# Optimization experiments

Measured on AMD Instinct MI355X. Metric: run time of the kernel, lower is better.

## Reference

```python
import jax, jax.numpy as jnp
import numpy as np

NUM_HEADS = 12
EPSILON = 1e-6
SCORE_SCALE = 1.0


def setup_inputs() -> dict:
    key = jax.random.key(0)
    ks = jax.random.split(key, 5)
    B, L, E = 2, 2048, 768
    x = jax.random.normal(ks[0], (B, L, E), dtype=jnp.float32)
    attention_mask = jnp.ones((B, L), dtype=jnp.int32)
    # linear params (lecun-ish scale)
    Wqkv = jax.random.normal(ks[1], (E, 3 * E), dtype=jnp.float32) / np.sqrt(E)
    bqkv = jnp.zeros((3 * E,), dtype=jnp.float32)
    Wout = jax.random.normal(ks[2], (E, E), dtype=jnp.float32) / np.sqrt(E)
    bout = jnp.zeros((E,), dtype=jnp.float32)
    return {"x": x, "attention_mask": attention_mask, "Wqkv": Wqkv,
            "bqkv": bqkv, "Wout": Wout, "bout": bout}


def reference(x, attention_mask, Wqkv, bqkv, Wout, bout):
    B, L, E = x.shape
    H = NUM_HEADS
    D = E // H
    qkv = x @ Wqkv + bqkv                      # [B,L,3E]
    q, k, v = jnp.split(qkv, 3, axis=-1)
    q = q.reshape(B, L, H, D).transpose(0, 2, 1, 3)  # [B,H,L,D]
    k = k.reshape(B, L, H, D).transpose(0, 2, 1, 3)
    v = v.reshape(B, L, H, D).transpose(0, 2, 1, 3)

    dot = jnp.einsum('bhid,bhjd->bhij', q, k)        # [B,H,L,L]
    q_sq = jnp.sum(q * q, axis=-1)[..., :, None]     # [B,H,L,1]
    k_sq = jnp.sum(k * k, axis=-1)[..., None, :]     # [B,H,1,L]
    scores = (dot * dot) / (q_sq + k_sq - 2.0 * dot + EPSILON)
    scores = scores * SCORE_SCALE

    pad = attention_mask[:, None, None, :]           # [B,1,1,L]
    scores = jnp.where(pad == 1, scores, jnp.finfo(scores.dtype).min)

    attn = jax.nn.softmax(scores, axis=-1)
    out = jnp.einsum('bhij,bhjd->bhid', attn, v)     # [B,H,L,D]
    out = out.transpose(0, 2, 1, 3).reshape(B, L, E)
    return out @ Wout + bout
```

## Files before the change

kernel.cpp:

```cpp
#include <hip/hip_runtime.h>
#include <hip/hip_bf16.h>
#include <cstdint>
#include <cstddef>


typedef __bf16 bf16_t;
typedef __bf16 bf16x8 __attribute__((ext_vector_type(8)));
typedef __bf16 bf16x4 __attribute__((ext_vector_type(4)));
typedef float floatx4 __attribute__((ext_vector_type(4)));

#define DEVI static __device__ __forceinline__

#define Bc 2
#define Lc 2048
#define Ec 768
#define Hc 12
#define Dc 64
#define N3c 2304
#define Mc 4096
#define ROWSc (Bc * Hc * Lc)

DEVI void glds16(const bf16_t* g, bf16_t* l) {
  __builtin_amdgcn_global_load_lds(
      (const __attribute__((address_space(1))) void*)g,
      (__attribute__((address_space(3))) void*)l, 16, 0, 0);
}


__global__ __launch_bounds__(256) void k_cvt(const float* __restrict__ in,
                                             bf16_t* __restrict__ out, int n) {
  int i = (blockIdx.x * 256 + threadIdx.x) * 4;
  if (i >= n) return;
  float4 v = *(const float4*)(in + i);
  bf16x4 o;
  o[0] = (bf16_t)v.x; o[1] = (bf16_t)v.y; o[2] = (bf16_t)v.z; o[3] = (bf16_t)v.w;
  *(bf16x4*)(out + i) = o;
}

__global__ __launch_bounds__(256) void k_tc(const float* __restrict__ in,
                                            bf16_t* __restrict__ out, int R, int C) {
  __shared__ float tile[32][33];
  int c0 = blockIdx.x * 32, r0 = blockIdx.y * 32;
  int tx = threadIdx.x, ty = threadIdx.y;
  #pragma unroll
  for (int i = 0; i < 32; i += 8)
    tile[ty + i][tx] = in[(size_t)(r0 + ty + i) * C + c0 + tx];
  __syncthreads();
  #pragma unroll
  for (int i = 0; i < 32; i += 8)
    out[(size_t)(c0 + ty + i) * R + r0 + tx] = (bf16_t)tile[tx][ty + i];
}


DEVI void gemm_core(const bf16_t* __restrict__ A, const bf16_t* __restrict__ Bt,
                    bf16_t* lA, bf16_t* lB, int m0, int n0, floatx4 (&acc)[4][4]) {
  const int tid = threadIdx.x, wave = tid >> 6, lane = tid & 63;
  const int wm = (wave >> 1) * 64, wn = (wave & 1) * 64;
  const int lrow = lane >> 2, lseg = lane & 3;
  const int quad = lane >> 4, r16 = lane & 15;
  for (int kk = 0; kk < 768; kk += 32) {
    glds16(A  + (size_t)(m0 + wave * 32      + lrow) * 768 + kk + lseg * 8, lA + (wave * 32) * 32);
    glds16(A  + (size_t)(m0 + wave * 32 + 16 + lrow) * 768 + kk + lseg * 8, lA + (wave * 32 + 16) * 32);
    glds16(Bt + (size_t)(n0 + wave * 32      + lrow) * 768 + kk + lseg * 8, lB + (wave * 32) * 32);
    glds16(Bt + (size_t)(n0 + wave * 32 + 16 + lrow) * 768 + kk + lseg * 8, lB + (wave * 32 + 16) * 32);
    __syncthreads();
    bf16x8 af[4], bv[4];
    #pragma unroll
    for (int mi = 0; mi < 4; mi++)
      af[mi] = *(const bf16x8*)(lA + (wm + mi * 16 + r16) * 32 + quad * 8);
    #pragma unroll
    for (int ni = 0; ni < 4; ni++)
      bv[ni] = *(const bf16x8*)(lB + (wn + ni * 16 + r16) * 32 + quad * 8);
    #pragma unroll
    for (int mi = 0; mi < 4; mi++)
      #pragma unroll
      for (int ni = 0; ni < 4; ni++)
        acc[mi][ni] = __builtin_amdgcn_mfma_f32_16x16x32_bf16(af[mi], bv[ni], acc[mi][ni], 0, 0, 0);
    __syncthreads();
  }
}

__global__ __launch_bounds__(256) void k_gemm_qkv(
    const bf16_t* __restrict__ A, const bf16_t* __restrict__ Bt,
    const float* __restrict__ bias,
    bf16_t* __restrict__ Qo, bf16_t* __restrict__ Ko, bf16_t* __restrict__ Vo) {
  __shared__ bf16_t lA[128 * 32];
  __shared__ bf16_t lB[128 * 32];
  const int m0 = blockIdx.y * 128, n0 = blockIdx.x * 128;
  const int tid = threadIdx.x, wave = tid >> 6, lane = tid & 63;
  const int wm = (wave >> 1) * 64, wn = (wave & 1) * 64;
  const int quad = lane >> 4, r16 = lane & 15;
  floatx4 acc[4][4] = {};
  gemm_core(A, Bt, lA, lB, m0, n0, acc);

  const int sec = n0 / 768;
  bf16_t* dst = (sec == 0) ? Qo : ((sec == 1) ? Ko : Vo);
  #pragma unroll
  for (int ni = 0; ni < 4; ni++) {
    const int n = n0 + wn + ni * 16 + r16;
    const int nn = n - sec * 768;
    const int h = nn >> 6, d = nn & 63;
    const float bvs = bias[n];
    #pragma unroll
    for (int mi = 0; mi < 4; mi++) {
      #pragma unroll
      for (int reg = 0; reg < 4; reg++) {
        const int m = m0 + wm + mi * 16 + quad * 4 + reg;
        const int b = m >> 11, l = m & 2047;
        const float v = acc[mi][ni][reg] + bvs;
        dst[(((size_t)(b * Hc + h)) * Lc + l) * Dc + d] = (bf16_t)v;
      }
    }
  }
}

__global__ __launch_bounds__(256) void k_gemm_out(
    const bf16_t* __restrict__ A, const bf16_t* __restrict__ Bt,
    const float* __restrict__ bias, float* __restrict__ out) {
  __shared__ bf16_t lA[128 * 32];
  __shared__ bf16_t lB[128 * 32];
  const int m0 = blockIdx.y * 128, n0 = blockIdx.x * 128;
  const int tid = threadIdx.x, wave = tid >> 6, lane = tid & 63;
  const int wm = (wave >> 1) * 64, wn = (wave & 1) * 64;
  const int quad = lane >> 4, r16 = lane & 15;
  floatx4 acc[4][4] = {};
  gemm_core(A, Bt, lA, lB, m0, n0, acc);
  #pragma unroll
  for (int ni = 0; ni < 4; ni++) {
    const int n = n0 + wn + ni * 16 + r16;
    const float bvs = bias[n];
    #pragma unroll
    for (int mi = 0; mi < 4; mi++) {
      #pragma unroll
      for (int reg = 0; reg < 4; reg++) {
        const int m = m0 + wm + mi * 16 + quad * 4 + reg;
        out[(size_t)m * Ec + n] = acc[mi][ni][reg] + bvs;
      }
    }
  }
}

__global__ __launch_bounds__(256) void k_sq(const bf16_t* __restrict__ Q,
                                            const bf16_t* __restrict__ K,
                                            const int* __restrict__ mask,
                                            float* __restrict__ qsq, float* __restrict__ ksq,
                                            float* __restrict__ mbias) {
  const int row = blockIdx.x * 256 + threadIdx.x;
  const bf16x8* q = (const bf16x8*)(Q + (size_t)row * 64);
  const bf16x8* k = (const bf16x8*)(K + (size_t)row * 64);
  float sq = 0.f, sk = 0.f;
  #pragma unroll
  for (int c = 0; c < 8; c++) {
    bf16x8 vq = q[c], vk = k[c];
    #pragma unroll
    for (int j = 0; j < 8; j++) {
      float a = (float)vq[j]; sq += a * a;
      float b = (float)vk[j]; sk += b * b;
    }
  }
  qsq[row] = sq;
  ksq[row] = sk + 1e-6f;
  const int bh = row >> 11, l = row & 2047;
  if (bh == 0 || bh == Hc) {
    const int b = bh / Hc;
    mbias[b * Lc + l] = (mask[b * Lc + l] == 1) ? 0.f : -1e30f;
  }
}

__global__ __launch_bounds__(256) void k_vt(const bf16_t* __restrict__ V,
                                            bf16_t* __restrict__ VT) {
  __shared__ bf16_t t[64][72];
  const int gid = blockIdx.x;
  const int bh = gid >> 5, j0 = (gid & 31) * 64;
  const int tid = threadIdx.x;
  const bf16_t* Vh = V + ((size_t)bh * Lc) * Dc;
  bf16_t* VTh = VT + ((size_t)bh * Dc) * Lc;
  #pragma unroll
  for (int it = 0; it < 2; ++it) {
    int c = tid + it * 256;
    int j = c >> 3, seg = c & 7;
    *(bf16x8*)&t[j][seg * 8] = *(const bf16x8*)(Vh + (size_t)(j0 + j) * 64 + seg * 8);
  }
  __syncthreads();
  #pragma unroll
  for (int it = 0; it < 2; ++it) {
    int c = tid + it * 256;
    int d = c >> 3, jseg = c & 7;
    bf16x8 o;
    #pragma unroll
    for (int u = 0; u < 8; u++) o[u] = t[jseg * 8 + u][d];
    *(bf16x8*)(VTh + (size_t)d * Lc + j0 + jseg * 8) = o;
  }
}

__global__ __launch_bounds__(256) void k_attn(
    const bf16_t* __restrict__ Q, const bf16_t* __restrict__ K,
    const bf16_t* __restrict__ VT, const float* __restrict__ qsq,
    const float* __restrict__ ksq, const float* __restrict__ mbias,
    bf16_t* __restrict__ AO) {
  __shared__ bf16_t lK[2][4096];
  __shared__ bf16_t lV[2][4096];
  __shared__ bf16_t lP[4][16 * 72];
  const int gid0 = blockIdx.x;
  const int gid = (gid0 & 7) * 96 + (gid0 >> 3);
  const int bh = gid >> 5, qt = gid & 31;
  const int b = bh / Hc;
  const int h = bh - b * Hc;
  const int tid = threadIdx.x, wave = tid >> 6, lane = tid & 63;
  const int quad = lane >> 4, r16 = lane & 15;
  const int q0 = qt * 64 + wave * 16;
  const bf16_t* Qh = Q + ((size_t)bh * Lc) * Dc;
  const bf16_t* Kh = K + ((size_t)bh * Lc) * Dc;
  const bf16_t* VTh = VT + ((size_t)bh * Dc) * Lc;
  const float* qsqh = qsq + bh * Lc;
  const float* ksqh = ksq + bh * Lc;
  const float* mbb = mbias + b * Lc;
  bf16_t* myP = &lP[wave][0];

  const int p0 = wave * 64 + lane;
  const int srow = p0 >> 3;
  const int sj = (p0 & 7) ^ (srow & 7);
  const bf16_t* kg0 = Kh + (size_t)srow * 64 + sj * 8;
  const bf16_t* kg1 = kg0 + 32 * 64;
  const bf16_t* vg0 = VTh + (size_t)srow * Lc + sj * 8;
  const bf16_t* vg1 = vg0 + 32 * Lc;
  const int ld0 = wave * 64 * 8, ld1 = (256 + wave * 64) * 8;

  const int sl0 = ((quad ^ (r16 & 7)) * 8);
  const int sl1 = sl0 ^ 32;

  bf16x8 qf0 = *(const bf16x8*)(Qh + (size_t)(q0 + r16) * 64 + quad * 8);
  bf16x8 qf1 = *(const bf16x8*)(Qh + (size_t)(q0 + r16) * 64 + 32 + quad * 8);
  const float qs = qsqh[q0 + r16];
  float mi = -1e30f, li = 0.f;
  floatx4 of[4] = {};

  glds16(kg0, &lK[0][ld0]);
  glds16(kg1, &lK[0][ld1]);
  glds16(vg0, &lV[0][ld0]);
  glds16(vg1, &lV[0][ld1]);
  kg0 += 4096; kg1 += 4096; vg0 += 64; vg1 += 64;
  __syncthreads();

  const int nt = Lc / 64;
  for (int t = 0; t < nt; t++) {
    const int cur = t & 1;
    if (t + 1 < nt) {
      const int nxt = cur ^ 1;
      glds16(kg0, &lK[nxt][ld0]);
      glds16(kg1, &lK[nxt][ld1]);
      glds16(vg0, &lV[nxt][ld0]);
      glds16(vg1, &lV[nxt][ld1]);
      kg0 += 4096; kg1 += 4096; vg0 += 64; vg1 += 64;
    }
    const int kt = t * 64;
    float4 ks4[4], mb4[4];
    #pragma unroll
    for (int c = 0; c < 4; c++) {
      ks4[c] = *(const float4*)(ksqh + kt + c * 16 + quad * 4);
      mb4[c] = *(const float4*)(mbb + kt + c * 16 + quad * 4);
    }
    floatx4 dot[4];
    #pragma unroll
    for (int c = 0; c < 4; c++) {
      const int rbase = (c * 16 + r16) * 64;
      bf16x8 kf0 = *(const bf16x8*)(&lK[cur][rbase + sl0]);
      bf16x8 kf1 = *(const bf16x8*)(&lK[cur][rbase + sl1]);
      floatx4 a = {};
      a = __builtin_amdgcn_mfma_f32_16x16x32_bf16(kf0, qf0, a, 0, 0, 0);
      a = __builtin_amdgcn_mfma_f32_16x16x32_bf16(kf1, qf1, a, 0, 0, 0);
      dot[c] = a;
    }
    float rmax = -1e30f;
    #pragma unroll
    for (int c = 0; c < 4; c++) {
      #pragma unroll
      for (int reg = 0; reg < 4; reg++) {
        const float dd = dot[c][reg];
        const float kss = ((const float*)&ks4[c])[reg];
        const float mbv = ((const float*)&mb4[c])[reg];
        const float den = __builtin_fmaf(dd, -2.f, qs + kss);
        const float sc = __builtin_fmaf((dd * 1.44269504f) * dd,
                                        __builtin_amdgcn_rcpf(den), mbv);
        dot[c][reg] = sc;
        rmax = fmaxf(rmax, sc);
      }
    }
    rmax = fmaxf(rmax, __shfl_xor(rmax, 16));
    rmax = fmaxf(rmax, __shfl_xor(rmax, 32));
    if (!__all(rmax <= mi + 11.5416f)) {
      const float mnew = fmaxf(mi, rmax);
      const float alpha = exp2f(mi - mnew);
      li *= alpha;
      #pragma unroll
      for (int t4 = 0; t4 < 4; t4++) {
        #pragma unroll
        for (int reg = 0; reg < 4; reg++) of[t4][reg] *= alpha;
      }
      mi = mnew;
    }
    float psum = 0.f;
    #pragma unroll
    for (int c = 0; c < 4; c++) {
      bf16x4 pk;
      #pragma unroll
      for (int reg = 0; reg < 4; reg++) {
        const float p = exp2f(dot[c][reg] - mi);
        psum += p;
        pk[reg] = (bf16_t)p;
      }
      *(bf16x4*)(myP + r16 * 72 + c * 16 + quad * 4) = pk;
    }
    psum += __shfl_xor(psum, 16);
    psum += __shfl_xor(psum, 32);
    li += psum;
    bf16x8 pf0 = *(const bf16x8*)(myP + r16 * 72 + quad * 8);
    bf16x8 pf1 = *(const bf16x8*)(myP + r16 * 72 + 32 + quad * 8);
    #pragma unroll
    for (int t4 = 0; t4 < 4; t4++) {
      const int rbase = (t4 * 16 + r16) * 64;
      bf16x8 vf0 = *(const bf16x8*)(&lV[cur][rbase + sl0]);
      bf16x8 vf1 = *(const bf16x8*)(&lV[cur][rbase + sl1]);
      of[t4] = __builtin_amdgcn_mfma_f32_16x16x32_bf16(vf0, pf0, of[t4], 0, 0, 0);
      of[t4] = __builtin_amdgcn_mfma_f32_16x16x32_bf16(vf1, pf1, of[t4], 0, 0, 0);
    }
    __syncthreads();
  }
  const float inv = (li > 0.f) ? __builtin_amdgcn_rcpf(li) : 0.f;
  bf16_t* aor = AO + ((size_t)(b * Lc + q0 + r16)) * Ec + h * 64;
  #pragma unroll
  for (int t4 = 0; t4 < 4; t4++) {
    bf16x4 o;
    #pragma unroll
    for (int reg = 0; reg < 4; reg++) o[reg] = (bf16_t)(of[t4][reg] * inv);
    *(bf16x4*)(aor + t4 * 16 + quad * 4) = o;
  }
}


extern "C" void kernel_launch(void* const* d_in, const int* in_sizes, int n_in,
                              void* d_out, int out_size, void* d_ws, size_t ws_size,
                              hipStream_t stream) {
  const float* x    = (const float*)d_in[0];
  const int*   mask = (const int*)d_in[1];
  const float* Wqkv = (const float*)d_in[2];
  const float* bqkv = (const float*)d_in[3];
  const float* Wout = (const float*)d_in[4];
  const float* bout = (const float*)d_in[5];
  float* out = (float*)d_out;

  auto al = [](size_t x) { return (x + 255) & ~(size_t)255; };
  char* ws = (char*)d_ws;
  size_t off = 0;
  auto carve = [&](size_t bytes) -> char* {
    char* p = ws + off;
    off += al(bytes);
    return p;
  };
  bf16_t* WoT = (bf16_t*)carve((size_t)Ec * Ec * 2);
  bf16_t* Qb  = (bf16_t*)carve((size_t)ROWSc * Dc * 2);
  bf16_t* Kb  = (bf16_t*)carve((size_t)ROWSc * Dc * 2);
  bf16_t* VTb = (bf16_t*)carve((size_t)ROWSc * Dc * 2);
  bf16_t* AOb = (bf16_t*)carve((size_t)Mc * Ec * 2);
  float*  qsq = (float*)carve((size_t)ROWSc * 4);
  float*  ksq = (float*)carve((size_t)ROWSc * 4);
  float*  mbias = (float*)carve((size_t)Bc * Lc * 4);
  const size_t uni = off;
  bf16_t* xb  = (bf16_t*)(ws + uni);
  bf16_t* WqT = (bf16_t*)(ws + uni + al((size_t)Mc * Ec * 2));
  bf16_t* Vb  = (bf16_t*)(ws + uni + al((size_t)Mc * Ec * 2) + al((size_t)N3c * Ec * 2));
  (void)in_sizes; (void)n_in; (void)out_size; (void)ws_size;

  k_cvt<<<(Mc * Ec / 4 + 255) / 256, 256, 0, stream>>>(x, xb, Mc * Ec);
  k_tc<<<dim3(N3c / 32, Ec / 32), dim3(32, 8), 0, stream>>>(Wqkv, WqT, Ec, N3c);
  k_tc<<<dim3(Ec / 32, Ec / 32), dim3(32, 8), 0, stream>>>(Wout, WoT, Ec, Ec);
  k_gemm_qkv<<<dim3(N3c / 128, Mc / 128), 256, 0, stream>>>(xb, WqT, bqkv, Qb, Kb, Vb);
  k_sq<<<ROWSc / 256, 256, 0, stream>>>(Qb, Kb, mask, qsq, ksq, mbias);
  k_vt<<<ROWSc / 64, 256, 0, stream>>>(Vb, VTb);
  k_attn<<<dim3(ROWSc / 64), 256, 0, stream>>>(Qb, Kb, VTb, qsq, ksq, mbias, AOb);
  k_gemm_out<<<dim3(Ec / 128, Mc / 128), 256, 0, stream>>>(AOb, WoT, bout, out);
}
```

Baseline: 219.4 us.

## Merge prep kernels, prefetch ksq/mask per tile, defer softmax reductions

Merges the x conversion and both weight transposes into one launch, and merges the squared-norm/mask kernel with the V transpose into another, cutting five launches to two. In the attention loop, the ksq and mask-bias loads for the next key tile are issued one iteration early. The row-max cross-lane shuffle now runs only inside the rescale branch, and the row-sum shuffle moves to after the loop. This trims per-iteration shuffles and load latency at the cost of extra registers, and the merged kernels use branching block roles.

Result: faster. 210.4 us (-4.1%).

```diff
diff --git a/kernel.cpp b/kernel.cpp
--- a/kernel.cpp
+++ b/kernel.cpp
@@ -26,22 +26,27 @@
       (__attribute__((address_space(3))) void*)l, 16, 0, 0);
 }
 
-
-__global__ __launch_bounds__(256) void k_cvt(const float* __restrict__ in,
-                                             bf16_t* __restrict__ out, int n) {
-  int i = (blockIdx.x * 256 + threadIdx.x) * 4;
-  if (i >= n) return;
-  float4 v = *(const float4*)(in + i);
-  bf16x4 o;
-  o[0] = (bf16_t)v.x; o[1] = (bf16_t)v.y; o[2] = (bf16_t)v.z; o[3] = (bf16_t)v.w;
-  *(bf16x4*)(out + i) = o;
-}
-
-__global__ __launch_bounds__(256) void k_tc(const float* __restrict__ in,
-                                            bf16_t* __restrict__ out, int R, int C) {
+__global__ __launch_bounds__(256) void k_prep(
+    const float* __restrict__ x, bf16_t* __restrict__ xb,
+    const float* __restrict__ Wqkv, bf16_t* __restrict__ WqT,
+    const float* __restrict__ Wout, bf16_t* __restrict__ WoT) {
   __shared__ float tile[32][33];
-  int c0 = blockIdx.x * 32, r0 = blockIdx.y * 32;
-  int tx = threadIdx.x, ty = threadIdx.y;
+  const int bid = blockIdx.x, tid = threadIdx.x;
+  if (bid < 3072) {
+    const int i = (bid * 256 + tid) * 4;
+    float4 v = *(const float4*)(x + i);
+    bf16x4 o;
+    o[0] = (bf16_t)v.x; o[1] = (bf16_t)v.y; o[2] = (bf16_t)v.z; o[3] = (bf16_t)v.w;
+    *(bf16x4*)(xb + i) = o;
+    return;
+  }
+  const float* in; bf16_t* out; int C, local;
+  if (bid < 4800) { local = bid - 3072; in = Wqkv; out = WqT; C = N3c; }
+  else            { local = bid - 4800; in = Wout; out = WoT; C = Ec;  }
+  const int R = Ec;
+  const int nbx = C / 32;
+  const int c0 = (local % nbx) * 32, r0 = (local / nbx) * 32;
+  const int tx = tid & 31, ty = tid >> 5;
   #pragma unroll
   for (int i = 0; i < 32; i += 8)
     tile[ty + i][tx] = in[(size_t)(r0 + ty + i) * C + c0 + tx];
@@ -140,46 +145,46 @@
   }
 }
 
-__global__ __launch_bounds__(256) void k_sq(const bf16_t* __restrict__ Q,
-                                            const bf16_t* __restrict__ K,
-                                            const int* __restrict__ mask,
-                                            float* __restrict__ qsq, float* __restrict__ ksq,
-                                            float* __restrict__ mbias) {
-  const int row = blockIdx.x * 256 + threadIdx.x;
-  const bf16x8* q = (const bf16x8*)(Q + (size_t)row * 64);
-  const bf16x8* k = (const bf16x8*)(K + (size_t)row * 64);
-  float sq = 0.f, sk = 0.f;
-  #pragma unroll
-  for (int c = 0; c < 8; c++) {
-    bf16x8 vq = q[c], vk = k[c];
-    #pragma unroll
-    for (int j = 0; j < 8; j++) {
-      float a = (float)vq[j]; sq += a * a;
-      float b = (float)vk[j]; sk += b * b;
-    }
-  }
-  qsq[row] = sq;
-  ksq[row] = sk + 1e-6f;
-  const int bh = row >> 11, l = row & 2047;
-  if (bh == 0 || bh == Hc) {
-    const int b = bh / Hc;
-    mbias[b * Lc + l] = (mask[b * Lc + l] == 1) ? 0.f : -1e30f;
-  }
-}
-
-__global__ __launch_bounds__(256) void k_vt(const bf16_t* __restrict__ V,
-                                            bf16_t* __restrict__ VT) {
-  __shared__ bf16_t t[64][72];
-  const int gid = blockIdx.x;
+__global__ __launch_bounds__(256) void k_prep2(
+    const bf16_t* __restrict__ Q, const bf16_t* __restrict__ K,
+    const int* __restrict__ mask,
+    float* __restrict__ qsq, float* __restrict__ ksq,
+    float* __restrict__ mbias,
+    const bf16_t* __restrict__ V, bf16_t* __restrict__ VT) {
+  __shared__ bf16_t tb[64][72];
+  const int bid = blockIdx.x, tid = threadIdx.x;
+  if (bid < 192) {
+    const int row = bid * 256 + tid;
+    const bf16x8* q = (const bf16x8*)(Q + (size_t)row * 64);
+    const bf16x8* k = (const bf16x8*)(K + (size_t)row * 64);
+    float sq = 0.f, sk = 0.f;
+    #pragma unroll
+    for (int c = 0; c < 8; c++) {
+      bf16x8 vq = q[c], vk = k[c];
+      #pragma unroll
+      for (int j = 0; j < 8; j++) {
+        float a = (float)vq[j]; sq += a * a;
+        float b = (float)vk[j]; sk += b * b;
+      }
+    }
+    qsq[row] = sq;
+    ksq[row] = sk + 1e-6f;
+    const int bh = row >> 11, l = row & 2047;
+    if (bh == 0 || bh == Hc) {
+      const int b = bh / Hc;
+      mbias[b * Lc + l] = (mask[b * Lc + l] == 1) ? 0.f : -1e30f;
+    }
+    return;
+  }
+  const int gid = bid - 192;
   const int bh = gid >> 5, j0 = (gid & 31) * 64;
-  const int tid = threadIdx.x;
   const bf16_t* Vh = V + ((size_t)bh * Lc) * Dc;
   bf16_t* VTh = VT + ((size_t)bh * Dc) * Lc;
   #pragma unroll
   for (int it = 0; it < 2; ++it) {
     int c = tid + it * 256;
     int j = c >> 3, seg = c & 7;
-    *(bf16x8*)&t[j][seg * 8] = *(const bf16x8*)(Vh + (size_t)(j0 + j) * 64 + seg * 8);
+    *(bf16x8*)&tb[j][seg * 8] = *(const bf16x8*)(Vh + (size_t)(j0 + j) * 64 + seg * 8);
   }
   __syncthreads();
   #pragma unroll
@@ -188,7 +193,7 @@
     int d = c >> 3, jseg = c & 7;
     bf16x8 o;
     #pragma unroll
-    for (int u = 0; u < 8; u++) o[u] = t[jseg * 8 + u][d];
+    for (int u = 0; u < 8; u++) o[u] = tb[jseg * 8 + u][d];
     *(bf16x8*)(VTh + (size_t)d * Lc + j0 + jseg * 8) = o;
   }
 }
@@ -232,7 +237,8 @@
   bf16x8 qf0 = *(const bf16x8*)(Qh + (size_t)(q0 + r16) * 64 + quad * 8);
   bf16x8 qf1 = *(const bf16x8*)(Qh + (size_t)(q0 + r16) * 64 + 32 + quad * 8);
   const float qs = qsqh[q0 + r16];
-  float mi = -1e30f, li = 0.f;
+  float mi = -1e30f;
+  float li = 0.f;
   floatx4 of[4] = {};
 
   glds16(kg0, &lK[0][ld0]);
@@ -240,12 +246,19 @@
   glds16(vg0, &lV[0][ld0]);
   glds16(vg1, &lV[0][ld1]);
   kg0 += 4096; kg1 += 4096; vg0 += 64; vg1 += 64;
+  float4 ks4[4], mb4[4];
+  #pragma unroll
+  for (int c = 0; c < 4; c++) {
+    ks4[c] = *(const float4*)(ksqh + c * 16 + quad * 4);
+    mb4[c] = *(const float4*)(mbb + c * 16 + quad * 4);
+  }
   __syncthreads();
 
   const int nt = Lc / 64;
   for (int t = 0; t < nt; t++) {
     const int cur = t & 1;
-    if (t + 1 < nt) {
+    const bool more = (t + 1 < nt);
+    if (more) {
       const int nxt = cur ^ 1;
       glds16(kg0, &lK[nxt][ld0]);
       glds16(kg1, &lK[nxt][ld1]);
@@ -253,12 +266,14 @@
       glds16(vg1, &lV[nxt][ld1]);
       kg0 += 4096; kg1 += 4096; vg0 += 64; vg1 += 64;
     }
-    const int kt = t * 64;
-    float4 ks4[4], mb4[4];
-    #pragma unroll
-    for (int c = 0; c < 4; c++) {
-      ks4[c] = *(const float4*)(ksqh + kt + c * 16 + quad * 4);
-      mb4[c] = *(const float4*)(mbb + kt + c * 16 + quad * 4);
+    float4 ks4n[4], mb4n[4];
+    if (more) {
+      const int ktn = (t + 1) * 64;
+      #pragma unroll
+      for (int c = 0; c < 4; c++) {
+        ks4n[c] = *(const float4*)(ksqh + ktn + c * 16 + quad * 4);
+        mb4n[c] = *(const float4*)(mbb + ktn + c * 16 + quad * 4);
+      }
     }
     floatx4 dot[4];
     #pragma unroll
@@ -286,10 +301,10 @@
         rmax = fmaxf(rmax, sc);
       }
     }
-    rmax = fmaxf(rmax, __shfl_xor(rmax, 16));
-    rmax = fmaxf(rmax, __shfl_xor(rmax, 32));
     if (!__all(rmax <= mi + 11.5416f)) {
-      const float mnew = fmaxf(mi, rmax);
+      float rg = fmaxf(rmax, __shfl_xor(rmax, 16));
+      rg = fmaxf(rg, __shfl_xor(rg, 32));
+      const float mnew = fmaxf(mi, rg);
       const float alpha = exp2f(mi - mnew);
       li *= alpha;
       #pragma unroll
@@ -311,8 +326,6 @@
       }
       *(bf16x4*)(myP + r16 * 72 + c * 16 + quad * 4) = pk;
     }
-    psum += __shfl_xor(psum, 16);
-    psum += __shfl_xor(psum, 32);
     li += psum;
     bf16x8 pf0 = *(const bf16x8*)(myP + r16 * 72 + quad * 8);
     bf16x8 pf1 = *(const bf16x8*)(myP + r16 * 72 + 32 + quad * 8);
@@ -324,8 +337,14 @@
       of[t4] = __builtin_amdgcn_mfma_f32_16x16x32_bf16(vf0, pf0, of[t4], 0, 0, 0);
       of[t4] = __builtin_amdgcn_mfma_f32_16x16x32_bf16(vf1, pf1, of[t4], 0, 0, 0);
     }
+    if (more) {
+      #pragma unroll
+      for (int c = 0; c < 4; c++) { ks4[c] = ks4n[c]; mb4[c] = mb4n[c]; }
+    }
     __syncthreads();
   }
+  li += __shfl_xor(li, 16);
+  li += __shfl_xor(li, 32);
   const float inv = (li > 0.f) ? __builtin_amdgcn_rcpf(li) : 0.f;
   bf16_t* aor = AO + ((size_t)(b * Lc + q0 + r16)) * Ec + h * 64;
   #pragma unroll
@@ -371,12 +390,9 @@
   bf16_t* Vb  = (bf16_t*)(ws + uni + al((size_t)Mc * Ec * 2) + al((size_t)N3c * Ec * 2));
   (void)in_sizes; (void)n_in; (void)out_size; (void)ws_size;
 
-  k_cvt<<<(Mc * Ec / 4 + 255) / 256, 256, 0, stream>>>(x, xb, Mc * Ec);
-  k_tc<<<dim3(N3c / 32, Ec / 32), dim3(32, 8), 0, stream>>>(Wqkv, WqT, Ec, N3c);
-  k_tc<<<dim3(Ec / 32, Ec / 32), dim3(32, 8), 0, stream>>>(Wout, WoT, Ec, Ec);
+  k_prep<<<5376, 256, 0, stream>>>(x, xb, Wqkv, WqT, Wout, WoT);
   k_gemm_qkv<<<dim3(N3c / 128, Mc / 128), 256, 0, stream>>>(xb, WqT, bqkv, Qb, Kb, Vb);
-  k_sq<<<ROWSc / 256, 256, 0, stream>>>(Qb, Kb, mask, qsq, ksq, mbias);
-  k_vt<<<ROWSc / 64, 256, 0, stream>>>(Vb, VTb);
+  k_prep2<<<960, 256, 0, stream>>>(Qb, Kb, mask, qsq, ksq, mbias, Vb, VTb);
   k_attn<<<dim3(ROWSc / 64), 256, 0, stream>>>(Qb, Kb, VTb, qsq, ksq, mbias, AOb);
   k_gemm_out<<<dim3(Ec / 128, Mc / 128), 256, 0, stream>>>(AOb, WoT, bout, out);
 }
```
